# Performance work log

Hardware: AMD Instinct MI355X
Metric: run time of the kernel (lower is better)

## Reference

```python
import jax, jax.numpy as jnp
import numpy as np

N_NODES = 50000
N_EDGES = 600000
N_GRAPHS = 500
HID = 128
N_LAYERS = 3
N_CLASSES = 10


def setup_inputs() -> dict:
    key = jax.random.key(0)
    ks = jax.random.split(key, 10)
    x = jax.random.normal(ks[0], (N_NODES, HID), dtype=jnp.float32)
    edge_attr = jax.random.normal(ks[1], (N_EDGES, 4), dtype=jnp.float32)
    edge_index = jax.random.randint(ks[2], (2, N_EDGES), 0, N_NODES, dtype=jnp.int32)
    batch = jnp.sort(jax.random.randint(ks[3], (N_NODES,), 0, N_GRAPHS, dtype=jnp.int32))
    s = 1.0 / np.sqrt(HID)
    Wl = jax.random.normal(ks[4], (N_LAYERS, HID, HID), dtype=jnp.float32) * s
    bl = jax.random.normal(ks[5], (N_LAYERS, HID), dtype=jnp.float32) * s
    Wr = jax.random.normal(ks[6], (N_LAYERS, HID, HID), dtype=jnp.float32) * s
    W1 = jax.random.normal(ks[7], (HID, HID), dtype=jnp.float32) * s
    b1 = jnp.zeros((HID,), dtype=jnp.float32)
    W2 = jax.random.normal(ks[8], (N_CLASSES, HID), dtype=jnp.float32) * s
    b2 = jnp.zeros((N_CLASSES,), dtype=jnp.float32)
    return {"x": x, "edge_attr": edge_attr, "edge_index": edge_index, "batch": batch,
            "Wl": Wl, "bl": bl, "Wr": Wr, "W1": W1, "b1": b1, "W2": W2, "b2": b2}


def _sage_conv(x, src, dst, Wl_i, bl_i, Wr_i):
    # mean aggregation of source-node features at target nodes (PyG SAGEConv)
    msg_sum = jax.ops.segment_sum(x[src], dst, num_segments=N_NODES)  # [N, H]
    cnt = jax.ops.segment_sum(jnp.ones((src.shape[0],), x.dtype), dst, num_segments=N_NODES)
    mean = msg_sum / jnp.maximum(cnt, 1.0)[:, None]
    return mean @ Wl_i.T + bl_i + x @ Wr_i.T


def reference(x, edge_attr, edge_index, batch, Wl, bl, Wr, W1, b1, W2, b2):
    # edge_attr is ignored by SAGEConv
    src, dst = edge_index[0], edge_index[1]
    for i in range(N_LAYERS):
        x = jax.nn.relu(_sage_conv(x, src, dst, Wl[i], bl[i], Wr[i]))
    # global_add_pool over graphs
    g = jax.ops.segment_sum(x, batch, num_segments=N_GRAPHS)  # [G, H]
    g = jax.nn.relu(g)
    # dropout p=0.5 is identity at inference
    h = jax.nn.relu(g @ W1.T + b1)
    logits = h @ W2.T + b2
    return jax.nn.log_softmax(logits, axis=1)
```

## Files before the change

kernel.cpp:

```cpp
#include <hip/hip_runtime.h>
#include <math.h>

#define HID 128
#define NCLS 10
#define MAXDEG 32

typedef __attribute__((ext_vector_type(8))) short frag8;
typedef __attribute__((ext_vector_type(8))) unsigned short u16x8;
typedef __attribute__((ext_vector_type(4))) float f32x4;

static __device__ __forceinline__ float relu_f(float v) { return v > 0.f ? v : 0.f; }

static __device__ __forceinline__ unsigned short f2bf(float f) {
    unsigned int u = __float_as_uint(f);
    u += 0x7fffu + ((u >> 16) & 1u);
    return (unsigned short)(u >> 16);
}
static __device__ __forceinline__ float bf2f(unsigned short u) {
    return __uint_as_float(((unsigned int)u) << 16);
}

static __device__ __forceinline__ void conv4(const float* __restrict__ in,
                                             unsigned short* __restrict__ out, int i) {
    float4 v = *(const float4*)&in[i * 4];
    ushort4 o;
    o.x = f2bf(v.x); o.y = f2bf(v.y); o.z = f2bf(v.z); o.w = f2bf(v.w);
    *(ushort4*)&out[i * 4] = o;
}

__global__ __launch_bounds__(256) void prep_kernel(const float* __restrict__ x, unsigned short* __restrict__ xb, int nx4,
                                                   const float* __restrict__ Wl, unsigned short* __restrict__ wlb, int nwl4,
                                                   const float* __restrict__ Wr, unsigned short* __restrict__ wrb, int nwr4,
                                                   int* __restrict__ deg, int ndeg4) {
    int i = blockIdx.x * blockDim.x + threadIdx.x;
    if (i < nx4) { conv4(x, xb, i); return; }
    i -= nx4;
    if (i < nwl4) { conv4(Wl, wlb, i); return; }
    i -= nwl4;
    if (i < nwr4) { conv4(Wr, wrb, i); return; }
    i -= nwr4;
    if (i < ndeg4) *(int4*)&deg[i * 4] = make_int4(0, 0, 0, 0);
}

__global__ void fill_kernel(const int* __restrict__ src, const int* __restrict__ dst,
                            int* __restrict__ deg, unsigned short* __restrict__ col, int nE) {
    int e = blockIdx.x * blockDim.x + threadIdx.x;
    if (e < nE) {
        int d = dst[e];
        int p = atomicAdd(&deg[d], 1);
        if (p < MAXDEG) col[(long)d * MAXDEG + p] = (unsigned short)src[e];
    }
}

__global__ __launch_bounds__(256) void agg_kernel(const unsigned short* __restrict__ xb,
                                                  const int* __restrict__ deg,
                                                  const unsigned short* __restrict__ col,
                                                  unsigned short* __restrict__ meanb, int nN) {
    int grp = threadIdx.x >> 4;
    int l16 = threadIdx.x & 15;
    int n = blockIdx.x * 16 + grp;
    bool valid = n < nN;
    int d = valid ? min(deg[n], MAXDEG) : 0;
    const unsigned short* cp = col + (long)n * MAXDEG;
    const long fo = (long)l16 * 8;

    float acc[8] = {0, 0, 0, 0, 0, 0, 0, 0};

    int p = 0;
    for (; p + 8 <= d; p += 8) {
        int s0 = cp[p],     s1 = cp[p + 1], s2 = cp[p + 2], s3 = cp[p + 3];
        int s4 = cp[p + 4], s5 = cp[p + 5], s6 = cp[p + 6], s7 = cp[p + 7];
        u16x8 v0 = *(const u16x8*)&xb[(long)s0 * HID + fo];
        u16x8 v1 = *(const u16x8*)&xb[(long)s1 * HID + fo];
        u16x8 v2 = *(const u16x8*)&xb[(long)s2 * HID + fo];
        u16x8 v3 = *(const u16x8*)&xb[(long)s3 * HID + fo];
        u16x8 v4 = *(const u16x8*)&xb[(long)s4 * HID + fo];
        u16x8 v5 = *(const u16x8*)&xb[(long)s5 * HID + fo];
        u16x8 v6 = *(const u16x8*)&xb[(long)s6 * HID + fo];
        u16x8 v7 = *(const u16x8*)&xb[(long)s7 * HID + fo];
#pragma unroll
        for (int j = 0; j < 8; ++j)
            acc[j] += ((bf2f(v0[j]) + bf2f(v1[j])) + (bf2f(v2[j]) + bf2f(v3[j]))) +
                      ((bf2f(v4[j]) + bf2f(v5[j])) + (bf2f(v6[j]) + bf2f(v7[j])));
    }
    if (p + 4 <= d) {
        int s0 = cp[p], s1 = cp[p + 1], s2 = cp[p + 2], s3 = cp[p + 3];
        u16x8 v0 = *(const u16x8*)&xb[(long)s0 * HID + fo];
        u16x8 v1 = *(const u16x8*)&xb[(long)s1 * HID + fo];
        u16x8 v2 = *(const u16x8*)&xb[(long)s2 * HID + fo];
        u16x8 v3 = *(const u16x8*)&xb[(long)s3 * HID + fo];
#pragma unroll
        for (int j = 0; j < 8; ++j)
            acc[j] += (bf2f(v0[j]) + bf2f(v1[j])) + (bf2f(v2[j]) + bf2f(v3[j]));
        p += 4;
    }
    if (p < d) {
        int s0 = cp[p];
        int s1 = cp[min(p + 1, MAXDEG - 1)];
        int s2 = cp[min(p + 2, MAXDEG - 1)];
        int s3 = cp[min(p + 3, MAXDEG - 1)];
        u16x8 v0 = *(const u16x8*)&xb[(long)s0 * HID + fo];
        u16x8 v1 = *(const u16x8*)&xb[(long)s1 * HID + fo];
        u16x8 v2 = *(const u16x8*)&xb[(long)s2 * HID + fo];
        u16x8 v3 = *(const u16x8*)&xb[(long)s3 * HID + fo];
#pragma unroll
        for (int j = 0; j < 8; ++j) acc[j] += bf2f(v0[j]);
        if (p + 1 < d) {
#pragma unroll
            for (int j = 0; j < 8; ++j) acc[j] += bf2f(v1[j]);
        }
        if (p + 2 < d) {
#pragma unroll
            for (int j = 0; j < 8; ++j) acc[j] += bf2f(v2[j]);
        }
        if (p + 3 < d) {
#pragma unroll
            for (int j = 0; j < 8; ++j) acc[j] += bf2f(v3[j]);
        }
    }

    if (valid) {
        float inv = 1.f / fmaxf((float)d, 1.f);
        u16x8 o;
#pragma unroll
        for (int j = 0; j < 8; ++j) o[j] = f2bf(acc[j] * inv);
        *(u16x8*)&meanb[(long)n * HID + fo] = o;
    }
}

__global__ __launch_bounds__(256) void gemm_kernel(const unsigned short* __restrict__ Ab,
                                                   const unsigned short* __restrict__ Xb,
                                                   const unsigned short* __restrict__ Wlb,
                                                   const unsigned short* __restrict__ Wrb,
                                                   const float* __restrict__ bl,
                                                   unsigned short* __restrict__ Yb, int nN) {
    int wave = threadIdx.x >> 6;
    int lane = threadIdx.x & 63;
    int l15 = lane & 15;
    int quad = lane >> 4;
    int r0 = blockIdx.x * 128 + wave * 32;

    f32x4 acc[2][8];
#pragma unroll
    for (int rt = 0; rt < 2; ++rt)
#pragma unroll
        for (int ct = 0; ct < 8; ++ct) acc[rt][ct] = (f32x4){0.f, 0.f, 0.f, 0.f};

#pragma unroll
    for (int ks = 0; ks < HID; ks += 32) {
        frag8 aM[2], aX[2];
#pragma unroll
        for (int rt = 0; rt < 2; ++rt) {
            long row = r0 + rt * 16 + l15;
            aM[rt] = *(const frag8*)&Ab[row * HID + ks + quad * 8];
            aX[rt] = *(const frag8*)&Xb[row * HID + ks + quad * 8];
        }
#pragma unroll
        for (int ct = 0; ct < 8; ++ct) {
            long nrow = ct * 16 + l15;
            frag8 bL = *(const frag8*)&Wlb[nrow * HID + ks + quad * 8];
            frag8 bR = *(const frag8*)&Wrb[nrow * HID + ks + quad * 8];
#pragma unroll
            for (int rt = 0; rt < 2; ++rt) {
                acc[rt][ct] = __builtin_amdgcn_mfma_f32_16x16x32_bf16(aM[rt], bL, acc[rt][ct], 0, 0, 0);
                acc[rt][ct] = __builtin_amdgcn_mfma_f32_16x16x32_bf16(aX[rt], bR, acc[rt][ct], 0, 0, 0);
            }
        }
    }

#pragma unroll
    for (int ct = 0; ct < 8; ++ct) {
        float bb = bl[ct * 16 + l15];
#pragma unroll
        for (int rt = 0; rt < 2; ++rt) {
#pragma unroll
            for (int reg = 0; reg < 4; ++reg) {
                int gm = r0 + rt * 16 + quad * 4 + reg;
                if (gm < nN) {
                    float v = relu_f(acc[rt][ct][reg] + bb);
                    Yb[(long)gm * HID + ct * 16 + l15] = f2bf(v);
                }
            }
        }
    }
}

__global__ __launch_bounds__(128) void poolmlp_kernel(const unsigned short* __restrict__ xb,
                                                      const int* __restrict__ batch, int nN,
                                                      const float* __restrict__ W1,
                                                      const float* __restrict__ b1,
                                                      const float* __restrict__ W2,
                                                      const float* __restrict__ b2,
                                                      float* __restrict__ out) {
    __shared__ float gs[HID];
    __shared__ float hs[HID];
    __shared__ float ls[NCLS];
    __shared__ float red[2];
    int gid = blockIdx.x;
    int j = threadIdx.x;

    int lo = 0, hi = nN;
    while (lo < hi) { int mid = (lo + hi) >> 1; if (batch[mid] < gid) lo = mid + 1; else hi = mid; }
    int s = lo;
    hi = nN;
    while (lo < hi) { int mid = (lo + hi) >> 1; if (batch[mid] < gid + 1) lo = mid + 1; else hi = mid; }
    int e = lo;

    float a0 = 0.f, a1 = 0.f, a2 = 0.f, a3 = 0.f;
    int n = s;
    for (; n + 4 <= e; n += 4) {
        a0 += bf2f(xb[(long)n * HID + j]);
        a1 += bf2f(xb[(long)(n + 1) * HID + j]);
        a2 += bf2f(xb[(long)(n + 2) * HID + j]);
        a3 += bf2f(xb[(long)(n + 3) * HID + j]);
    }
    for (; n < e; ++n) a0 += bf2f(xb[(long)n * HID + j]);
    gs[j] = relu_f((a0 + a1) + (a2 + a3));
    __syncthreads();

    float acc = b1[j];
#pragma unroll 8
    for (int k = 0; k < HID; ++k) acc += gs[k] * W1[j * HID + k];
    hs[j] = relu_f(acc);
    __syncthreads();
    if (j < NCLS) {
        float lg = b2[j];
#pragma unroll 8
        for (int k = 0; k < HID; ++k) lg += hs[k] * W2[j * HID + k];
        ls[j] = lg;
    }
    __syncthreads();
    if (j == 0) {
        float m = ls[0];
        for (int c = 1; c < NCLS; ++c) m = fmaxf(m, ls[c]);
        float sum = 0.f;
        for (int c = 0; c < NCLS; ++c) sum += expf(ls[c] - m);
        red[0] = m;
        red[1] = logf(sum);
    }
    __syncthreads();
    if (j < NCLS) out[gid * NCLS + j] = ls[j] - red[0] - red[1];
}


extern "C" void kernel_launch(void* const* d_in, const int* in_sizes, int n_in,
                              void* d_out, int out_size, void* d_ws, size_t ws_size,
                              hipStream_t stream) {
    const float* x_in  = (const float*)d_in[0];
    const int*   eidx  = (const int*)d_in[2];
    const int*   batch = (const int*)d_in[3];
    const float* Wl    = (const float*)d_in[4];
    const float* bl    = (const float*)d_in[5];
    const float* Wr    = (const float*)d_in[6];
    const float* W1    = (const float*)d_in[7];
    const float* b1    = (const float*)d_in[8];
    const float* W2    = (const float*)d_in[9];
    const float* b2    = (const float*)d_in[10];
    float* out = (float*)d_out;

    const int nN = in_sizes[0] / HID;
    const int nE = in_sizes[2] / 2;
    const int nG = out_size / NCLS;
    const int nWl = in_sizes[4];
    const int nWr = in_sizes[6];
    const int nNp = (nN + 127) & ~127;
    const int nTiles = nNp / 128;

    const int* src = eidx;
    const int* dst = eidx + nE;

    char* p = (char*)d_ws;
    auto carve = [&](size_t bytes) {
        char* r = p;
        p += (bytes + 255) & ~(size_t)255;
        return r;
    };
    unsigned short* xb    = (unsigned short*)carve((size_t)nNp * HID * 2);
    unsigned short* meanb = (unsigned short*)carve((size_t)nNp * HID * 2);
    unsigned short* yb0   = (unsigned short*)carve((size_t)nNp * HID * 2);
    unsigned short* yb1   = (unsigned short*)carve((size_t)nNp * HID * 2);
    unsigned short* wlb   = (unsigned short*)carve((size_t)nWl * 2);
    unsigned short* wrb   = (unsigned short*)carve((size_t)nWr * 2);
    int*   deg    = (int*)carve((size_t)nN * 4);
    unsigned short* col = (unsigned short*)carve((size_t)nN * MAXDEG * 2);
    (void)ws_size; (void)n_in;

    const int nx4 = nN * HID / 4, nwl4 = nWl / 4, nwr4 = nWr / 4, ndeg4 = (nN + 3) / 4;
    const int prep_total = nx4 + nwl4 + nwr4 + ndeg4;
    prep_kernel<<<(prep_total + 255) / 256, 256, 0, stream>>>(
        x_in, xb, nx4, Wl, wlb, nwl4, Wr, wrb, nwr4, deg, ndeg4);

    fill_kernel<<<(nE + 255) / 256, 256, 0, stream>>>(src, dst, deg, col, nE);

    const unsigned short* xcur = xb;
    unsigned short* bufs[2] = {yb0, yb1};
    for (int l = 0; l < 3; ++l) {
        agg_kernel<<<(nN + 15) / 16, 256, 0, stream>>>(xcur, deg, col, meanb, nN);
        gemm_kernel<<<nTiles, 256, 0, stream>>>(
            meanb, xcur, wlb + (size_t)l * HID * HID, wrb + (size_t)l * HID * HID,
            bl + (size_t)l * HID, bufs[l & 1], nN);
        xcur = bufs[l & 1];
    }

    poolmlp_kernel<<<nG, 128, 0, stream>>>(xcur, batch, nN, W1, b1, W2, b2, out);
}
```

Baseline: 308.0 us.

## Fuse whole GNN pipeline into one cooperative persistent kernel with grid syncs

Replaces the sequence of prep, fill, three aggregate/GEMM pairs and pool-MLP launches with a single cooperative kernel. Phases are separated by grid-wide barriers and each phase loops over work in grid-stride fashion. The goal is to remove the per-launch overhead of the roughly nine launches. In exchange, occupancy is capped by the cooperative grid size, and grid.sync plus the tail effects of persistent scheduling add their own cost. The old multi-kernel path is kept as a fallback if the cooperative launch fails.

```diff
diff --git a/kernel.cpp b/kernel.cpp
--- a/kernel.cpp
+++ b/kernel.cpp
@@ -1,5 +1,8 @@
 #include <hip/hip_runtime.h>
+#include <hip/hip_cooperative_groups.h>
 #include <math.h>
+
+namespace cg = cooperative_groups;
 
 #define HID 128
 #define NCLS 10
@@ -26,6 +29,239 @@
     ushort4 o;
     o.x = f2bf(v.x); o.y = f2bf(v.y); o.z = f2bf(v.z); o.w = f2bf(v.w);
     *(ushort4*)&out[i * 4] = o;
+}
+
+__global__ __launch_bounds__(256, 4) void mega_kernel(
+    const float* __restrict__ x_in,
+    const int* __restrict__ src, const int* __restrict__ dst,
+    const int* __restrict__ batch,
+    const float* __restrict__ Wl, const float* __restrict__ bl,
+    const float* __restrict__ Wr,
+    const float* __restrict__ W1, const float* __restrict__ b1,
+    const float* __restrict__ W2, const float* __restrict__ b2,
+    float* __restrict__ out,
+    unsigned short* __restrict__ xb, unsigned short* __restrict__ meanb,
+    unsigned short* __restrict__ yb0, unsigned short* __restrict__ yb1,
+    unsigned short* __restrict__ wlb, unsigned short* __restrict__ wrb,
+    int* __restrict__ deg, unsigned short* __restrict__ col,
+    int nN, int nE, int nG, int nTiles)
+{
+    cg::grid_group grid = cg::this_grid();
+    const int tid = threadIdx.x;
+    const int gthreads = gridDim.x * blockDim.x;
+    const int gtid = blockIdx.x * blockDim.x + tid;
+
+    {
+        const int nx4 = nN * HID / 4;
+        const int nw4 = 3 * HID * HID / 4;
+        const int total0 = nx4 + 2 * nw4 + nN;
+        for (int i = gtid; i < total0; i += gthreads) {
+            int k = i;
+            if (k < nx4) { conv4(x_in, xb, k); continue; }
+            k -= nx4;
+            if (k < nw4) { conv4(Wl, wlb, k); continue; }
+            k -= nw4;
+            if (k < nw4) { conv4(Wr, wrb, k); continue; }
+            k -= nw4;
+            deg[k] = 0;
+        }
+    }
+    grid.sync();
+
+    for (int e = gtid; e < nE; e += gthreads) {
+        int d = dst[e];
+        int p = atomicAdd(&deg[d], 1);
+        if (p < MAXDEG) col[(long)d * MAXDEG + p] = (unsigned short)src[e];
+    }
+    grid.sync();
+
+    const unsigned short* xcur = xb;
+    unsigned short* bufs[2] = {yb0, yb1};
+    for (int l = 0; l < 3; ++l) {
+        {
+            const int grp = tid >> 4;
+            const int l16 = tid & 15;
+            const long fo = (long)l16 * 8;
+            for (int n = blockIdx.x * 16 + grp; n < nN; n += gridDim.x * 16) {
+                int d = min(deg[n], MAXDEG);
+                const unsigned short* cp = col + (long)n * MAXDEG;
+                float acc[8] = {0, 0, 0, 0, 0, 0, 0, 0};
+                int p = 0;
+                for (; p + 8 <= d; p += 8) {
+                    int s0 = cp[p],     s1 = cp[p + 1], s2 = cp[p + 2], s3 = cp[p + 3];
+                    int s4 = cp[p + 4], s5 = cp[p + 5], s6 = cp[p + 6], s7 = cp[p + 7];
+                    u16x8 v0 = *(const u16x8*)&xcur[(long)s0 * HID + fo];
+                    u16x8 v1 = *(const u16x8*)&xcur[(long)s1 * HID + fo];
+                    u16x8 v2 = *(const u16x8*)&xcur[(long)s2 * HID + fo];
+                    u16x8 v3 = *(const u16x8*)&xcur[(long)s3 * HID + fo];
+                    u16x8 v4 = *(const u16x8*)&xcur[(long)s4 * HID + fo];
+                    u16x8 v5 = *(const u16x8*)&xcur[(long)s5 * HID + fo];
+                    u16x8 v6 = *(const u16x8*)&xcur[(long)s6 * HID + fo];
+                    u16x8 v7 = *(const u16x8*)&xcur[(long)s7 * HID + fo];
+#pragma unroll
+                    for (int j = 0; j < 8; ++j)
+                        acc[j] += ((bf2f(v0[j]) + bf2f(v1[j])) + (bf2f(v2[j]) + bf2f(v3[j]))) +
+                                  ((bf2f(v4[j]) + bf2f(v5[j])) + (bf2f(v6[j]) + bf2f(v7[j])));
+                }
+                if (p + 4 <= d) {
+                    int s0 = cp[p], s1 = cp[p + 1], s2 = cp[p + 2], s3 = cp[p + 3];
+                    u16x8 v0 = *(const u16x8*)&xcur[(long)s0 * HID + fo];
+                    u16x8 v1 = *(const u16x8*)&xcur[(long)s1 * HID + fo];
+                    u16x8 v2 = *(const u16x8*)&xcur[(long)s2 * HID + fo];
+                    u16x8 v3 = *(const u16x8*)&xcur[(long)s3 * HID + fo];
+#pragma unroll
+                    for (int j = 0; j < 8; ++j)
+                        acc[j] += (bf2f(v0[j]) + bf2f(v1[j])) + (bf2f(v2[j]) + bf2f(v3[j]));
+                    p += 4;
+                }
+                if (p < d) {
+                    int s0 = cp[p];
+                    int s1 = cp[min(p + 1, MAXDEG - 1)];
+                    int s2 = cp[min(p + 2, MAXDEG - 1)];
+                    int s3 = cp[min(p + 3, MAXDEG - 1)];
+                    u16x8 v0 = *(const u16x8*)&xcur[(long)s0 * HID + fo];
+                    u16x8 v1 = *(const u16x8*)&xcur[(long)s1 * HID + fo];
+                    u16x8 v2 = *(const u16x8*)&xcur[(long)s2 * HID + fo];
+                    u16x8 v3 = *(const u16x8*)&xcur[(long)s3 * HID + fo];
+#pragma unroll
+                    for (int j = 0; j < 8; ++j) acc[j] += bf2f(v0[j]);
+                    if (p + 1 < d) {
+#pragma unroll
+                        for (int j = 0; j < 8; ++j) acc[j] += bf2f(v1[j]);
+                    }
+                    if (p + 2 < d) {
+#pragma unroll
+                        for (int j = 0; j < 8; ++j) acc[j] += bf2f(v2[j]);
+                    }
+                    if (p + 3 < d) {
+#pragma unroll
+                        for (int j = 0; j < 8; ++j) acc[j] += bf2f(v3[j]);
+                    }
+                }
+                float inv = 1.f / fmaxf((float)d, 1.f);
+                u16x8 o;
+#pragma unroll
+                for (int j = 0; j < 8; ++j) o[j] = f2bf(acc[j] * inv);
+                *(u16x8*)&meanb[(long)n * HID + fo] = o;
+            }
+        }
+        grid.sync();
+
+        {
+            const unsigned short* Wlb_l = wlb + (size_t)l * HID * HID;
+            const unsigned short* Wrb_l = wrb + (size_t)l * HID * HID;
+            const float* bl_l = bl + (size_t)l * HID;
+            unsigned short* Yb = bufs[l & 1];
+            const int wave = tid >> 6;
+            const int lane = tid & 63;
+            const int l15 = lane & 15;
+            const int quad = lane >> 4;
+            for (int tile = blockIdx.x; tile < nTiles; tile += gridDim.x) {
+                int r0 = tile * 128 + wave * 32;
+                f32x4 acc[2][8];
+#pragma unroll
+                for (int rt = 0; rt < 2; ++rt)
+#pragma unroll
+                    for (int ct = 0; ct < 8; ++ct) acc[rt][ct] = (f32x4){0.f, 0.f, 0.f, 0.f};
+#pragma unroll
+                for (int ks = 0; ks < HID; ks += 32) {
+                    frag8 aM[2], aX[2];
+#pragma unroll
+                    for (int rt = 0; rt < 2; ++rt) {
+                        long row = r0 + rt * 16 + l15;
+                        aM[rt] = *(const frag8*)&meanb[row * HID + ks + quad * 8];
+                        aX[rt] = *(const frag8*)&xcur[row * HID + ks + quad * 8];
+                    }
+#pragma unroll
+                    for (int ct = 0; ct < 8; ++ct) {
+                        long nrow = ct * 16 + l15;
+                        frag8 bL = *(const frag8*)&Wlb_l[nrow * HID + ks + quad * 8];
+                        frag8 bR = *(const frag8*)&Wrb_l[nrow * HID + ks + quad * 8];
+#pragma unroll
+                        for (int rt = 0; rt < 2; ++rt) {
+                            acc[rt][ct] = __builtin_amdgcn_mfma_f32_16x16x32_bf16(aM[rt], bL, acc[rt][ct], 0, 0, 0);
+                            acc[rt][ct] = __builtin_amdgcn_mfma_f32_16x16x32_bf16(aX[rt], bR, acc[rt][ct], 0, 0, 0);
+                        }
+                    }
+                }
+#pragma unroll
+                for (int ct = 0; ct < 8; ++ct) {
+                    float bb = bl_l[ct * 16 + l15];
+#pragma unroll
+                    for (int rt = 0; rt < 2; ++rt) {
+#pragma unroll
+                        for (int reg = 0; reg < 4; ++reg) {
+                            int gm = r0 + rt * 16 + quad * 4 + reg;
+                            if (gm < nN) {
+                                float v = relu_f(acc[rt][ct][reg] + bb);
+                                Yb[(long)gm * HID + ct * 16 + l15] = f2bf(v);
+                            }
+                        }
+                    }
+                }
+            }
+        }
+        xcur = bufs[l & 1];
+        grid.sync();
+    }
+
+    {
+        __shared__ float gs[2][HID];
+        __shared__ float hs[2][HID];
+        __shared__ float ls[2][NCLS];
+        __shared__ float red[2][2];
+        const int half = tid >> 7;
+        const int j = tid & 127;
+        const int step = gridDim.x * 2;
+        const int iters = (nG + step - 1) / step;
+        for (int it = 0; it < iters; ++it) {
+            int gid = it * step + blockIdx.x * 2 + half;
+            bool act = gid < nG;
+            int s = 0, e = 0;
+            if (act) {
+                int lo = 0, hi = nN;
+                while (lo < hi) { int mid = (lo + hi) >> 1; if (batch[mid] < gid) lo = mid + 1; else hi = mid; }
+                s = lo;
+                hi = nN;
+                while (lo < hi) { int mid = (lo + hi) >> 1; if (batch[mid] < gid + 1) lo = mid + 1; else hi = mid; }
+                e = lo;
+            }
+            float a0 = 0.f, a1 = 0.f, a2 = 0.f, a3 = 0.f;
+            int n = s;
+            for (; n + 4 <= e; n += 4) {
+                a0 += bf2f(xcur[(long)n * HID + j]);
+                a1 += bf2f(xcur[(long)(n + 1) * HID + j]);
+                a2 += bf2f(xcur[(long)(n + 2) * HID + j]);
+                a3 += bf2f(xcur[(long)(n + 3) * HID + j]);
+            }
+            for (; n < e; ++n) a0 += bf2f(xcur[(long)n * HID + j]);
+            gs[half][j] = relu_f((a0 + a1) + (a2 + a3));
+            __syncthreads();
+            float acc = b1[j];
+#pragma unroll 8
+            for (int k = 0; k < HID; ++k) acc += gs[half][k] * W1[j * HID + k];
+            hs[half][j] = relu_f(acc);
+            __syncthreads();
+            if (j < NCLS) {
+                float lg = b2[j];
+#pragma unroll 8
+                for (int k = 0; k < HID; ++k) lg += hs[half][k] * W2[j * HID + k];
+                ls[half][j] = lg;
+            }
+            __syncthreads();
+            if (j == 0) {
+                float m = ls[half][0];
+                for (int c = 1; c < NCLS; ++c) m = fmaxf(m, ls[half][c]);
+                float sum = 0.f;
+                for (int c = 0; c < NCLS; ++c) sum += expf(ls[half][c] - m);
+                red[half][0] = m;
+                red[half][1] = logf(sum);
+            }
+            __syncthreads();
+            if (act && j < NCLS) out[gid * NCLS + j] = ls[half][j] - red[half][0] - red[half][1];
+            __syncthreads();
+        }
+    }
 }
 
 __global__ __launch_bounds__(256) void prep_kernel(const float* __restrict__ x, unsigned short* __restrict__ xb, int nx4,
@@ -63,9 +299,7 @@
     int d = valid ? min(deg[n], MAXDEG) : 0;
     const unsigned short* cp = col + (long)n * MAXDEG;
     const long fo = (long)l16 * 8;
-
     float acc[8] = {0, 0, 0, 0, 0, 0, 0, 0};
-
     int p = 0;
     for (; p + 8 <= d; p += 8) {
         int s0 = cp[p],     s1 = cp[p + 1], s2 = cp[p + 2], s3 = cp[p + 3];
@@ -118,7 +352,6 @@
             for (int j = 0; j < 8; ++j) acc[j] += bf2f(v3[j]);
         }
     }
-
     if (valid) {
         float inv = 1.f / fmaxf((float)d, 1.f);
         u16x8 o;
@@ -139,13 +372,11 @@
     int l15 = lane & 15;
     int quad = lane >> 4;
     int r0 = blockIdx.x * 128 + wave * 32;
-
     f32x4 acc[2][8];
 #pragma unroll
     for (int rt = 0; rt < 2; ++rt)
 #pragma unroll
         for (int ct = 0; ct < 8; ++ct) acc[rt][ct] = (f32x4){0.f, 0.f, 0.f, 0.f};
-
 #pragma unroll
     for (int ks = 0; ks < HID; ks += 32) {
         frag8 aM[2], aX[2];
@@ -167,7 +398,6 @@
             }
         }
     }
-
 #pragma unroll
     for (int ct = 0; ct < 8; ++ct) {
         float bb = bl[ct * 16 + l15];
@@ -198,14 +428,12 @@
     __shared__ float red[2];
     int gid = blockIdx.x;
     int j = threadIdx.x;
-
     int lo = 0, hi = nN;
     while (lo < hi) { int mid = (lo + hi) >> 1; if (batch[mid] < gid) lo = mid + 1; else hi = mid; }
     int s = lo;
     hi = nN;
     while (lo < hi) { int mid = (lo + hi) >> 1; if (batch[mid] < gid + 1) lo = mid + 1; else hi = mid; }
     int e = lo;
-
     float a0 = 0.f, a1 = 0.f, a2 = 0.f, a3 = 0.f;
     int n = s;
     for (; n + 4 <= e; n += 4) {
@@ -217,7 +445,6 @@
     for (; n < e; ++n) a0 += bf2f(xb[(long)n * HID + j]);
     gs[j] = relu_f((a0 + a1) + (a2 + a3));
     __syncthreads();
-
     float acc = b1[j];
 #pragma unroll 8
     for (int k = 0; k < HID; ++k) acc += gs[k] * W1[j * HID + k];
@@ -285,13 +512,40 @@
     unsigned short* col = (unsigned short*)carve((size_t)nN * MAXDEG * 2);
     (void)ws_size; (void)n_in;
 
+    int dev = 0, numCU = 0, occ = 0;
+    hipGetDevice(&dev);
+    hipDeviceGetAttribute(&numCU, hipDeviceAttributeMultiprocessorCount, dev);
+    hipError_t occ_err = hipOccupancyMaxActiveBlocksPerMultiprocessor(&occ, mega_kernel, 256, 0);
+    if (occ_err != hipSuccess || occ < 1) occ = 1;
+    if (numCU < 1) numCU = 256;
+    if (occ > 4) occ = 4;
+    int gridBlocks = occ * numCU;
+
+    const float* a_x = x_in; const int* a_src = src; const int* a_dst = dst;
+    const int* a_batch = batch;
+    const float* a_Wl = Wl; const float* a_bl = bl; const float* a_Wr = Wr;
+    const float* a_W1 = W1; const float* a_b1 = b1;
+    const float* a_W2 = W2; const float* a_b2 = b2;
+    float* a_out = out;
+    unsigned short* a_xb = xb; unsigned short* a_meanb = meanb;
+    unsigned short* a_yb0 = yb0; unsigned short* a_yb1 = yb1;
+    unsigned short* a_wlb = wlb; unsigned short* a_wrb = wrb;
+    int* a_deg = deg; unsigned short* a_col = col;
+    int a_nN = nN, a_nE = nE, a_nG = nG, a_nTiles = nTiles;
+    void* args[] = {&a_x, &a_src, &a_dst, &a_batch, &a_Wl, &a_bl, &a_Wr,
+                    &a_W1, &a_b1, &a_W2, &a_b2, &a_out,
+                    &a_xb, &a_meanb, &a_yb0, &a_yb1, &a_wlb, &a_wrb,
+                    &a_deg, &a_col, &a_nN, &a_nE, &a_nG, &a_nTiles};
+
+    hipError_t err = hipLaunchCooperativeKernel(mega_kernel, dim3(gridBlocks), dim3(256),
+                                                args, 0u, stream);
+    if (err == hipSuccess) return;
+
     const int nx4 = nN * HID / 4, nwl4 = nWl / 4, nwr4 = nWr / 4, ndeg4 = (nN + 3) / 4;
     const int prep_total = nx4 + nwl4 + nwr4 + ndeg4;
     prep_kernel<<<(prep_total + 255) / 256, 256, 0, stream>>>(
         x_in, xb, nx4, Wl, wlb, nwl4, Wr, wrb, nwr4, deg, ndeg4);
-
     fill_kernel<<<(nE + 255) / 256, 256, 0, stream>>>(src, dst, deg, col, nE);
-
     const unsigned short* xcur = xb;
     unsigned short* bufs[2] = {yb0, yb1};
     for (int l = 0; l < 3; ++l) {
@@ -301,6 +555,5 @@
             bl + (size_t)l * HID, bufs[l & 1], nN);
         xcur = bufs[l & 1];
     }
-
     poolmlp_kernel<<<nG, 128, 0, stream>>>(xcur, batch, nN, W1, b1, W2, b2, out);
 }
```

New measurement: 959.7 us. +211.6%, slower.
